# Kernel optimization log

Hardware: AMD Instinct MI355X
Metric: run time of the kernel (lower is better)

## Reference

```python
import jax, jax.numpy as jnp
import numpy as np

NUM_SPARSE = 26
VOCAB = 100000
EMB = 64
B = 2048
DENSE = 13
NUM_FEA = NUM_SPARSE + 1  # 26 embeddings + bottom-MLP output


def _xavier(key, shape):
    fan_in, fan_out = shape[0], shape[1]
    lim = jnp.sqrt(6.0 / (fan_in + fan_out))
    return jax.random.uniform(key, shape, jnp.float32, -lim, lim)


def setup_inputs() -> dict:
    key = jax.random.key(0)
    ks = jax.random.split(key, 20)
    inp = {
        "dense": jax.random.normal(ks[0], (B, DENSE), jnp.float32),
        "cat_idx": jax.random.randint(ks[1], (B, NUM_SPARSE), 0, VOCAB, jnp.int32),
        # stacked EmbeddingBag tables (all same vocab -> one [26, V, 64] tensor)
        "tables": _xavier(ks[2], (VOCAB, EMB))[None] * jnp.ones((NUM_SPARSE, 1, 1), jnp.float32) * 0
                  + jax.random.normal(ks[3], (NUM_SPARSE, VOCAB, EMB), jnp.float32) * 0.01,
        # bottom MLP: 13 -> 512 -> 256 -> 64
        "bw0": _xavier(ks[4], (DENSE, 512)), "bb0": jnp.zeros((512,), jnp.float32),
        "bw1": _xavier(ks[5], (512, 256)),   "bb1": jnp.zeros((256,), jnp.float32),
        "bw2": _xavier(ks[6], (256, EMB)),   "bb2": jnp.zeros((EMB,), jnp.float32),
        # top MLP: 415 -> 1024 -> 512 -> 256 -> 1
        "tw0": _xavier(ks[7], (EMB + NUM_FEA * (NUM_FEA - 1) // 2, 1024)), "tb0": jnp.zeros((1024,), jnp.float32),
        "tw1": _xavier(ks[8], (1024, 512)),  "tb1": jnp.zeros((512,), jnp.float32),
        "tw2": _xavier(ks[9], (512, 256)),   "tb2": jnp.zeros((256,), jnp.float32),
        "tw3": _xavier(ks[10], (256, 1)),    "tb3": jnp.zeros((1,), jnp.float32),
    }
    return inp


def reference(dense, cat_idx, tables, bw0, bb0, bw1, bb1, bw2, bb2,
              tw0, tb0, tw1, tb1, tw2, tb2, tw3, tb3):
    # bottom MLP on dense features -> [B, EMB]
    h = jax.nn.relu(dense @ bw0 + bb0)
    h = jax.nn.relu(h @ bw1 + bb1)
    bot = jax.nn.relu(h @ bw2 + bb2)

    # EmbeddingBag (single index per bag, sum mode == plain gather): [B, 26, EMB]
    feat_ids = jnp.arange(NUM_SPARSE)[None, :]  # [1, 26]
    emb = tables[feat_ids, cat_idx]             # [B, 26, EMB]

    # dot interaction: batched Gram matrix then lower-triangular gather
    T = jnp.concatenate([bot[:, None, :], emb], axis=1)  # [B, 27, EMB]
    Z = jnp.einsum("bif,bjf->bij", T, T)                  # [B, 27, 27]
    li, lj = np.tril_indices(NUM_FEA, k=-1)               # 351 pairs
    Zflat = Z[:, li, lj]                                  # [B, 351]

    R = jnp.concatenate([bot, Zflat], axis=1)             # [B, 415]

    # top MLP
    r = jax.nn.relu(R @ tw0 + tb0)
    r = jax.nn.relu(r @ tw1 + tb1)
    r = jax.nn.relu(r @ tw2 + tb2)
    out = jax.nn.sigmoid(r @ tw3 + tb3)                   # [B, 1]
    return out
```

## Files before the change

kernel.cpp:

```cpp
#include <hip/hip_runtime.h>
#include <hip/hip_bf16.h>


#define BATCH 2048
#define VOCAB 100000
#define EMB 64
#define NSPARSE 26
#define NFEA 27
#define NPAIR 351
#define RLD 448

typedef __attribute__((ext_vector_type(8))) __bf16 bf16x8;
typedef __attribute__((ext_vector_type(4))) float f32x4;
typedef __hip_bfloat16 bf16;

#define GLOAD16(g, l)                                                          \
    __builtin_amdgcn_global_load_lds(                                          \
        (const __attribute__((address_space(1))) unsigned int*)(g),            \
        (__attribute__((address_space(3))) unsigned int*)(l), 16, 0, 0)

template<int BK>
__device__ __forceinline__ int swz(int row, int s) {
    return (BK == 64) ? (s ^ (row & 7)) : (s ^ ((row >> 1) & 3));
}

template<int BK, int WR, int WC, int MREP, int NREP, bool DENSEPAD>
__global__ __launch_bounds__(256) void gemm_bf16(
    const void* __restrict__ Araw,
    const bf16* __restrict__ Wt,
    const float* __restrict__ bias,
    bf16* __restrict__ C,
    int M, int N, int K, int ldC)
{
    constexpr int BM    = WR * MREP * 16;
    constexpr int BN    = WC * NREP * 16;
    constexpr int ROWB  = BK * 2;
    constexpr int SLOTS = BK / 8;
    constexpr int KKS   = BK / 32;
    constexpr int PA    = BM * SLOTS / 256;
    constexpr int PB    = BN * SLOTS / 256;

    __shared__ __align__(16) bf16 As[BM * BK];
    __shared__ __align__(16) bf16 Bs[BN * BK];

    const int t   = threadIdx.x;
    const int nbn = N / BN;
    const int bm  = blockIdx.x / nbn;
    const int bn  = blockIdx.x % nbn;
    const int row0 = bm * BM, n0 = bn * BN;

    const int wid  = t >> 6, lane = t & 63;
    const int wr   = wid / WC, wc = wid % WC;
    const int lr   = lane & 15;
    const int q    = lane >> 4;

    const int sslot = t % SLOTS;

    const bf16* Ab[PA];
    const bf16* Bb[PB];
#pragma unroll
    for (int p = 0; p < PA; ++p) {
        const int r = (p * 256 + t) / SLOTS;
        if (!DENSEPAD)
            Ab[p] = (const bf16*)Araw + (size_t)(row0 + r) * K +
                    swz<BK>(r, sslot) * 8;
    }
#pragma unroll
    for (int p = 0; p < PB; ++p) {
        const int r = (p * 256 + t) / SLOTS;
        Bb[p] = Wt + (size_t)(n0 + r) * K + swz<BK>(r, sslot) * 8;
    }

    f32x4 acc[MREP][NREP] = {};

    for (int k0 = 0; k0 < K; k0 += BK) {
        if constexpr (DENSEPAD) {
            const float* Df = (const float*)Araw;
#pragma unroll
            for (int idx = t; idx < BM * 32; idx += 256) {
                const int r = idx >> 5, c = idx & 31;
                const float v = (c < 13) ? Df[(size_t)(row0 + r) * 13 + c] : 0.f;
                As[r * 32 + swz<BK>(r, c >> 3) * 8 + (c & 7)] =
                    __float2bfloat16(v);
            }
        } else {
#pragma unroll
            for (int p = 0; p < PA; ++p)
                GLOAD16(Ab[p] + k0, (char*)As + (p * 256 + t) * 16);
        }
#pragma unroll
        for (int p = 0; p < PB; ++p)
            GLOAD16(Bb[p] + k0, (char*)Bs + (p * 256 + t) * 16);
        __syncthreads();

        bf16x8 af[KKS][MREP], bfr[KKS][NREP];
#pragma unroll
        for (int kk = 0; kk < KKS; ++kk) {
#pragma unroll
            for (int m = 0; m < MREP; ++m) {
                const int r = wr * MREP * 16 + 16 * m + lr;
                af[kk][m] = *(const bf16x8*)((const char*)As + r * ROWB +
                                             swz<BK>(r, kk * 4 + q) * 16);
            }
#pragma unroll
            for (int n = 0; n < NREP; ++n) {
                const int r = wc * NREP * 16 + 16 * n + lr;
                bfr[kk][n] = *(const bf16x8*)((const char*)Bs + r * ROWB +
                                              swz<BK>(r, kk * 4 + q) * 16);
            }
        }
#pragma unroll
        for (int kk = 0; kk < KKS; ++kk)
#pragma unroll
            for (int m = 0; m < MREP; ++m)
#pragma unroll
                for (int n = 0; n < NREP; ++n)
                    acc[m][n] = __builtin_amdgcn_mfma_f32_16x16x32_bf16(
                        af[kk][m], bfr[kk][n], acc[m][n], 0, 0, 0);
        __syncthreads();
    }

#pragma unroll
    for (int n = 0; n < NREP; ++n) {
        const int col = n0 + wc * NREP * 16 + 16 * n + lr;
        const float bv = bias[col];
#pragma unroll
        for (int m = 0; m < MREP; ++m) {
#pragma unroll
            for (int i = 0; i < 4; ++i) {
                const int row = row0 + wr * MREP * 16 + 16 * m + q * 4 + i;
                float v = acc[m][n][i] + bv;
                v = fmaxf(v, 0.f);
                C[(size_t)row * ldC + col] = __float2bfloat16(v);
            }
        }
    }
}

struct WConvArgs {
    const float* src[6];
    bf16*        dst[6];
    int K[6], N[6], Kp[6], t0[7];
};

__global__ __launch_bounds__(256) void wconv_kernel(WConvArgs a)
{
    __shared__ float Ts[32][33];
    int w = 0;
    while (w < 5 && (int)blockIdx.x >= a.t0[w + 1]) ++w;
    const int rel = blockIdx.x - a.t0[w];
    const int K = a.K[w], N = a.N[w], Kp = a.Kp[w];
    const int nbn = N >> 5;
    const int tk = rel / nbn, tn = rel % nbn;
    const int tx = threadIdx.x & 31, ty = threadIdx.x >> 5;

    const float* src = a.src[w];
    bf16* dst = a.dst[w];

#pragma unroll
    for (int rr = 0; rr < 4; ++rr) {
        const int k = tk * 32 + ty + rr * 8;
        const int n = tn * 32 + tx;
        Ts[ty + rr * 8][tx] = (k < K) ? src[(size_t)k * N + n] : 0.f;
    }
    __syncthreads();
#pragma unroll
    for (int rr = 0; rr < 4; ++rr) {
        const int n = tn * 32 + ty + rr * 8;
        const int kp = tk * 32 + tx;
        dst[(size_t)n * Kp + kp] = __float2bfloat16(Ts[tx][ty + rr * 8]);
    }
}

__global__ __launch_bounds__(256) void interact_kernel(
    const bf16* __restrict__ h1,
    const bf16* __restrict__ bw2t,
    const float* __restrict__ bb2,
    const int* __restrict__ cat_idx,
    const float* __restrict__ tables,
    bf16* __restrict__ R)
{
    __shared__ float T[2][NFEA][EMB + 1];
    __shared__ bf16  h1s[2][256];

    const int b0 = blockIdx.x * 2;
    const int t  = threadIdx.x;

    if (t < 64) {
        const int r = t >> 5, c = (t & 31) * 8;
        *(bf16x8*)&h1s[r][c] =
            *(const bf16x8*)&h1[(size_t)(b0 + r) * 256 + c];
    }

    for (int l = t; l < 2 * NSPARSE * 16; l += 256) {
        const int r   = l / (NSPARSE * 16);
        const int rem = l % (NSPARSE * 16);
        const int j   = rem >> 4, c = (rem & 15) * 4;
        const int idx = cat_idx[(b0 + r) * NSPARSE + j];
        const float4 v =
            *(const float4*)&tables[((size_t)j * VOCAB + idx) * EMB + c];
        float* dst = &T[r][j + 1][c];
        dst[0] = v.x; dst[1] = v.y; dst[2] = v.z; dst[3] = v.w;
    }

    for (int z = t; z < 2 * (RLD - 415); z += 256) {
        const int r = z / (RLD - 415), c = z % (RLD - 415);
        R[(size_t)(b0 + r) * RLD + 415 + c] = __float2bfloat16(0.f);
    }
    __syncthreads();

    if (t < 128) {
        const int r = t >> 6, n = t & 63;
        float s = bb2[n];
        const bf16* wrow = bw2t + (size_t)n * 256;
#pragma unroll 8
        for (int k = 0; k < 256; k += 8) {
            const bf16x8 hv = *(const bf16x8*)&h1s[r][k];
            const bf16x8 wv = *(const bf16x8*)&wrow[k];
#pragma unroll
            for (int u = 0; u < 8; ++u)
                s += (float)hv[u] * (float)wv[u];
        }
        s = fmaxf(s, 0.f);
        T[r][0][n] = s;
        R[(size_t)(b0 + r) * RLD + n] = __float2bfloat16(s);
    }
    __syncthreads();

    for (int task = t; task < 2 * NPAIR; task += 256) {
        const int r = task / NPAIR, p = task % NPAIR;
        int i = (int)((1.0f + sqrtf(1.0f + 8.0f * (float)p)) * 0.5f);
        while (i * (i - 1) / 2 > p) --i;
        while ((i + 1) * i / 2 <= p) ++i;
        const int j = p - i * (i - 1) / 2;
        float s = 0.f;
#pragma unroll 16
        for (int k = 0; k < EMB; ++k) s += T[r][i][k] * T[r][j][k];
        R[(size_t)(b0 + r) * RLD + EMB + p] = __float2bfloat16(s);
    }
}

__global__ __launch_bounds__(256) void top3_kernel(
    const bf16* __restrict__ A, const float* __restrict__ w,
    const float* __restrict__ bias, float* __restrict__ out)
{
    const int gid  = blockIdx.x * 256 + threadIdx.x;
    const int row  = gid >> 6;
    const int lane = gid & 63;

    const bf16* arow = A + (size_t)row * 256;
    float s = 0.f;
#pragma unroll
    for (int k = lane; k < 256; k += 64)
        s += __bfloat162float(arow[k]) * w[k];
#pragma unroll
    for (int off = 32; off; off >>= 1) s += __shfl_down(s, off);
    if (lane == 0) out[row] = 1.f / (1.f + expf(-(s + bias[0])));
}

extern "C" void kernel_launch(void* const* d_in, const int* in_sizes, int n_in,
                              void* d_out, int out_size, void* d_ws, size_t ws_size,
                              hipStream_t stream)
{
    const float* dense   = (const float*)d_in[0];
    const int*   cat_idx = (const int*)  d_in[1];
    const float* tables  = (const float*)d_in[2];
    const float* bw0 = (const float*)d_in[3];
    const float* bb0 = (const float*)d_in[4];
    const float* bw1 = (const float*)d_in[5];
    const float* bb1 = (const float*)d_in[6];
    const float* bw2 = (const float*)d_in[7];
    const float* bb2 = (const float*)d_in[8];
    const float* tw0 = (const float*)d_in[9];
    const float* tb0 = (const float*)d_in[10];
    const float* tw1 = (const float*)d_in[11];
    const float* tb1 = (const float*)d_in[12];
    const float* tw2 = (const float*)d_in[13];
    const float* tb2 = (const float*)d_in[14];
    const float* tw3 = (const float*)d_in[15];
    const float* tb3 = (const float*)d_in[16];

    bf16* p = (bf16*)d_ws;
    bf16* h0   = p; p += (size_t)BATCH * 512;
    bf16* h1   = p; p += (size_t)BATCH * 256;
    bf16* R    = p; p += (size_t)BATCH * RLD;
    bf16* r0   = p; p += (size_t)BATCH * 1024;
    bf16* r1   = p; p += (size_t)BATCH * 512;
    bf16* r2   = p; p += (size_t)BATCH * 256;
    bf16* bw0t = p; p += 512 * 32;
    bf16* bw1t = p; p += 256 * 512;
    bf16* bw2t = p; p += 64 * 256;
    bf16* tw0t = p; p += 1024 * RLD;
    bf16* tw1t = p; p += 512 * 1024;
    bf16* tw2t = p; p += 256 * 512;
    float* out = (float*)d_out;

    WConvArgs wa;
    wa.src[0] = bw0;  wa.dst[0] = bw0t; wa.K[0] = 13;   wa.N[0] = 512;  wa.Kp[0] = 32;
    wa.src[1] = bw1;  wa.dst[1] = bw1t; wa.K[1] = 512;  wa.N[1] = 256;  wa.Kp[1] = 512;
    wa.src[2] = bw2;  wa.dst[2] = bw2t; wa.K[2] = 256;  wa.N[2] = 64;   wa.Kp[2] = 256;
    wa.src[3] = tw0;  wa.dst[3] = tw0t; wa.K[3] = 415;  wa.N[3] = 1024; wa.Kp[3] = RLD;
    wa.src[4] = tw1;  wa.dst[4] = tw1t; wa.K[4] = 1024; wa.N[4] = 512;  wa.Kp[4] = 1024;
    wa.src[5] = tw2;  wa.dst[5] = tw2t; wa.K[5] = 512;  wa.N[5] = 256;  wa.Kp[5] = 512;
    int tiles = 0;
    for (int w = 0; w < 6; ++w) {
        wa.t0[w] = tiles;
        tiles += (wa.Kp[w] >> 5) * (wa.N[w] >> 5);
    }
    wa.t0[6] = tiles;

    wconv_kernel<<<tiles, 256, 0, stream>>>(wa);

    gemm_bf16<32, 2, 2, 2, 2, true ><<<(BATCH / 64) * (512 / 64), 256, 0, stream>>>(
        dense, bw0t, bb0, h0, BATCH, 512, 32, 512);
    gemm_bf16<64, 2, 2, 2, 2, false><<<(BATCH / 64) * (256 / 64), 256, 0, stream>>>(
        h0, bw1t, bb1, h1, BATCH, 256, 512, 256);

    interact_kernel<<<BATCH / 2, 256, 0, stream>>>(
        h1, bw2t, bb2, cat_idx, tables, R);

    gemm_bf16<64, 4, 1, 2, 4, false><<<(BATCH / 128) * (1024 / 64), 256, 0, stream>>>(
        R, tw0t, tb0, r0, BATCH, 1024, RLD, 1024);
    gemm_bf16<64, 2, 2, 2, 2, false><<<(BATCH / 64) * (512 / 64), 256, 0, stream>>>(
        r0, tw1t, tb1, r1, BATCH, 512, 1024, 512);
    gemm_bf16<64, 2, 2, 2, 2, false><<<(BATCH / 64) * (256 / 64), 256, 0, stream>>>(
        r1, tw2t, tb2, r2, BATCH, 256, 512, 256);
    top3_kernel<<<BATCH / 4, 256, 0, stream>>>(r2, tw3, tb3, out);
}
```

Before: 70.29 us.

## Triple-buffer GEMM loads, move bottom layer to GEMM, split interaction per row

The bf16 GEMM now uses a three-stage LDS ring with async global-to-LDS loads and manual vmcnt waits, so loads for later k-steps overlap MFMA work. The last bottom-MLP layer moves out of the interaction kernel into a separate MFMA GEMM that writes straight into R. The interaction kernel now handles one batch row per block with coalesced per-feature gathers. The first top-layer GEMM switches to 64x64 tiles. This adds LDS use and one more launch, and the hardcoded vmcnt assumes exactly four loads per thread.

```diff
diff --git a/kernel.cpp b/kernel.cpp
--- a/kernel.cpp
+++ b/kernel.cpp
@@ -40,9 +40,6 @@
     constexpr int PA    = BM * SLOTS / 256;
     constexpr int PB    = BN * SLOTS / 256;
 
-    __shared__ __align__(16) bf16 As[BM * BK];
-    __shared__ __align__(16) bf16 Bs[BN * BK];
-
     const int t   = threadIdx.x;
     const int nbn = N / BN;
     const int bm  = blockIdx.x / nbn;
@@ -53,44 +50,27 @@
     const int wr   = wid / WC, wc = wid % WC;
     const int lr   = lane & 15;
     const int q    = lane >> 4;
-
     const int sslot = t % SLOTS;
 
-    const bf16* Ab[PA];
-    const bf16* Bb[PB];
-#pragma unroll
-    for (int p = 0; p < PA; ++p) {
-        const int r = (p * 256 + t) / SLOTS;
-        if (!DENSEPAD)
-            Ab[p] = (const bf16*)Araw + (size_t)(row0 + r) * K +
-                    swz<BK>(r, sslot) * 8;
-    }
-#pragma unroll
-    for (int p = 0; p < PB; ++p) {
-        const int r = (p * 256 + t) / SLOTS;
-        Bb[p] = Wt + (size_t)(n0 + r) * K + swz<BK>(r, sslot) * 8;
-    }
-
     f32x4 acc[MREP][NREP] = {};
 
-    for (int k0 = 0; k0 < K; k0 += BK) {
-        if constexpr (DENSEPAD) {
-            const float* Df = (const float*)Araw;
-#pragma unroll
-            for (int idx = t; idx < BM * 32; idx += 256) {
-                const int r = idx >> 5, c = idx & 31;
-                const float v = (c < 13) ? Df[(size_t)(row0 + r) * 13 + c] : 0.f;
-                As[r * 32 + swz<BK>(r, c >> 3) * 8 + (c & 7)] =
-                    __float2bfloat16(v);
-            }
-        } else {
-#pragma unroll
-            for (int p = 0; p < PA; ++p)
-                GLOAD16(Ab[p] + k0, (char*)As + (p * 256 + t) * 16);
-        }
-#pragma unroll
-        for (int p = 0; p < PB; ++p)
-            GLOAD16(Bb[p] + k0, (char*)Bs + (p * 256 + t) * 16);
+    if constexpr (DENSEPAD) {
+        __shared__ __align__(16) bf16 As[BM * BK];
+        __shared__ __align__(16) bf16 Bs[BN * BK];
+
+        const float* Df = (const float*)Araw;
+#pragma unroll
+        for (int p = 0; p < PB; ++p) {
+            const int r = (p * 256 + t) / SLOTS;
+            GLOAD16(Wt + (size_t)(n0 + r) * K + swz<BK>(r, sslot) * 8,
+                    (char*)Bs + (p * 256 + t) * 16);
+        }
+#pragma unroll
+        for (int idx = t; idx < BM * 32; idx += 256) {
+            const int r = idx >> 5, c = idx & 31;
+            const float v = (c < 13) ? Df[(size_t)(row0 + r) * 13 + c] : 0.f;
+            As[r * 32 + swz<BK>(r, c >> 3) * 8 + (c & 7)] = __float2bfloat16(v);
+        }
         __syncthreads();
 
         bf16x8 af[KKS][MREP], bfr[KKS][NREP];
@@ -117,7 +97,77 @@
                 for (int n = 0; n < NREP; ++n)
                     acc[m][n] = __builtin_amdgcn_mfma_f32_16x16x32_bf16(
                         af[kk][m], bfr[kk][n], acc[m][n], 0, 0, 0);
-        __syncthreads();
+    } else {
+        static_assert(PA + PB == 4, "vmcnt immediate assumes 4 loads/thread");
+        __shared__ __align__(16) bf16 As[3][BM * BK];
+        __shared__ __align__(16) bf16 Bs[3][BN * BK];
+
+        const bf16* Ab[PA];
+        const bf16* Bb[PB];
+#pragma unroll
+        for (int p = 0; p < PA; ++p) {
+            const int r = (p * 256 + t) / SLOTS;
+            Ab[p] = (const bf16*)Araw + (size_t)(row0 + r) * K +
+                    swz<BK>(r, sslot) * 8;
+        }
+#pragma unroll
+        for (int p = 0; p < PB; ++p) {
+            const int r = (p * 256 + t) / SLOTS;
+            Bb[p] = Wt + (size_t)(n0 + r) * K + swz<BK>(r, sslot) * 8;
+        }
+
+        const int nsteps = K / BK;
+        auto stage = [&](int s) {
+            const int buf = s % 3;
+            const int k0  = (s < nsteps ? s : nsteps - 1) * BK;
+#pragma unroll
+            for (int p = 0; p < PA; ++p)
+                GLOAD16(Ab[p] + k0, (char*)As[buf] + (p * 256 + t) * 16);
+#pragma unroll
+            for (int p = 0; p < PB; ++p)
+                GLOAD16(Bb[p] + k0, (char*)Bs[buf] + (p * 256 + t) * 16);
+        };
+
+        stage(0);
+        stage(1);
+
+        for (int ks = 0; ks < nsteps; ++ks) {
+            stage(ks + 2);
+
+            asm volatile("s_waitcnt vmcnt(8)" ::: "memory");
+            __builtin_amdgcn_s_barrier();
+            __builtin_amdgcn_sched_barrier(0);
+
+            const int buf = ks % 3;
+            bf16x8 af[KKS][MREP], bfr[KKS][NREP];
+#pragma unroll
+            for (int kk = 0; kk < KKS; ++kk) {
+#pragma unroll
+                for (int m = 0; m < MREP; ++m) {
+                    const int r = wr * MREP * 16 + 16 * m + lr;
+                    af[kk][m] = *(const bf16x8*)((const char*)As[buf] + r * ROWB +
+                                                 swz<BK>(r, kk * 4 + q) * 16);
+                }
+#pragma unroll
+                for (int n = 0; n < NREP; ++n) {
+                    const int r = wc * NREP * 16 + 16 * n + lr;
+                    bfr[kk][n] = *(const bf16x8*)((const char*)Bs[buf] + r * ROWB +
+                                                  swz<BK>(r, kk * 4 + q) * 16);
+                }
+            }
+#pragma unroll
+            for (int kk = 0; kk < KKS; ++kk)
+#pragma unroll
+                for (int m = 0; m < MREP; ++m)
+#pragma unroll
+                    for (int n = 0; n < NREP; ++n)
+                        acc[m][n] = __builtin_amdgcn_mfma_f32_16x16x32_bf16(
+                            af[kk][m], bfr[kk][n], acc[m][n], 0, 0, 0);
+
+            asm volatile("s_waitcnt lgkmcnt(0)" ::: "memory");
+            __builtin_amdgcn_s_barrier();
+            __builtin_amdgcn_sched_barrier(0);
+        }
     }
 
 #pragma unroll
@@ -173,70 +223,39 @@
 }
 
 __global__ __launch_bounds__(256) void interact_kernel(
-    const bf16* __restrict__ h1,
-    const bf16* __restrict__ bw2t,
-    const float* __restrict__ bb2,
-    const int* __restrict__ cat_idx,
-    const float* __restrict__ tables,
+    const int* __restrict__ cat_idx, const float* __restrict__ tables,
     bf16* __restrict__ R)
 {
-    __shared__ float T[2][NFEA][EMB + 1];
-    __shared__ bf16  h1s[2][256];
-
-    const int b0 = blockIdx.x * 2;
-    const int t  = threadIdx.x;
-
-    if (t < 64) {
-        const int r = t >> 5, c = (t & 31) * 8;
-        *(bf16x8*)&h1s[r][c] =
-            *(const bf16x8*)&h1[(size_t)(b0 + r) * 256 + c];
-    }
-
-    for (int l = t; l < 2 * NSPARSE * 16; l += 256) {
-        const int r   = l / (NSPARSE * 16);
-        const int rem = l % (NSPARSE * 16);
-        const int j   = rem >> 4, c = (rem & 15) * 4;
-        const int idx = cat_idx[(b0 + r) * NSPARSE + j];
-        const float4 v =
-            *(const float4*)&tables[((size_t)j * VOCAB + idx) * EMB + c];
-        float* dst = &T[r][j + 1][c];
-        dst[0] = v.x; dst[1] = v.y; dst[2] = v.z; dst[3] = v.w;
-    }
-
-    for (int z = t; z < 2 * (RLD - 415); z += 256) {
-        const int r = z / (RLD - 415), c = z % (RLD - 415);
-        R[(size_t)(b0 + r) * RLD + 415 + c] = __float2bfloat16(0.f);
+    __shared__ float T[NFEA][EMB + 1];
+
+    const int b    = blockIdx.x;
+    const int t    = threadIdx.x;
+    const int g    = t >> 6;
+    const int lane = t & 63;
+    bf16* Rrow = R + (size_t)b * RLD;
+
+    for (int f = g; f < NFEA; f += 4) {
+        if (f == 0) {
+            T[0][lane] = __bfloat162float(Rrow[lane]);
+        } else {
+            const int j   = f - 1;
+            const int idx = cat_idx[b * NSPARSE + j];
+            T[f][lane] = tables[((size_t)j * VOCAB + idx) * EMB + lane];
+        }
     }
     __syncthreads();
 
-    if (t < 128) {
-        const int r = t >> 6, n = t & 63;
-        float s = bb2[n];
-        const bf16* wrow = bw2t + (size_t)n * 256;
-#pragma unroll 8
-        for (int k = 0; k < 256; k += 8) {
-            const bf16x8 hv = *(const bf16x8*)&h1s[r][k];
-            const bf16x8 wv = *(const bf16x8*)&wrow[k];
-#pragma unroll
-            for (int u = 0; u < 8; ++u)
-                s += (float)hv[u] * (float)wv[u];
-        }
-        s = fmaxf(s, 0.f);
-        T[r][0][n] = s;
-        R[(size_t)(b0 + r) * RLD + n] = __float2bfloat16(s);
-    }
-    __syncthreads();
-
-    for (int task = t; task < 2 * NPAIR; task += 256) {
-        const int r = task / NPAIR, p = task % NPAIR;
+    if (t < RLD - 415) Rrow[415 + t] = __float2bfloat16(0.f);
+
+    for (int p = t; p < NPAIR; p += 256) {
         int i = (int)((1.0f + sqrtf(1.0f + 8.0f * (float)p)) * 0.5f);
         while (i * (i - 1) / 2 > p) --i;
         while ((i + 1) * i / 2 <= p) ++i;
         const int j = p - i * (i - 1) / 2;
         float s = 0.f;
 #pragma unroll 16
-        for (int k = 0; k < EMB; ++k) s += T[r][i][k] * T[r][j][k];
-        R[(size_t)(b0 + r) * RLD + EMB + p] = __float2bfloat16(s);
+        for (int k = 0; k < EMB; ++k) s += T[i][k] * T[j][k];
+        Rrow[EMB + p] = __float2bfloat16(s);
     }
 }
 
@@ -315,11 +334,12 @@
         dense, bw0t, bb0, h0, BATCH, 512, 32, 512);
     gemm_bf16<64, 2, 2, 2, 2, false><<<(BATCH / 64) * (256 / 64), 256, 0, stream>>>(
         h0, bw1t, bb1, h1, BATCH, 256, 512, 256);
-
-    interact_kernel<<<BATCH / 2, 256, 0, stream>>>(
-        h1, bw2t, bb2, cat_idx, tables, R);
-
-    gemm_bf16<64, 4, 1, 2, 4, false><<<(BATCH / 128) * (1024 / 64), 256, 0, stream>>>(
+    gemm_bf16<64, 2, 2, 2, 2, false><<<(BATCH / 64) * (64 / 64), 256, 0, stream>>>(
+        h1, bw2t, bb2, R, BATCH, 64, 256, RLD);
+
+    interact_kernel<<<BATCH, 256, 0, stream>>>(cat_idx, tables, R);
+
+    gemm_bf16<64, 2, 2, 2, 2, false><<<(BATCH / 64) * (1024 / 64), 256, 0, stream>>>(
         R, tw0t, tb0, r0, BATCH, 1024, RLD, 1024);
     gemm_bf16<64, 2, 2, 2, 2, false><<<(BATCH / 64) * (512 / 64), 256, 0, stream>>>(
         r0, tw1t, tb1, r1, BATCH, 512, 1024, 512);
```

Result: faster. 66.97 us (-4.7%).

## Fuse weight conversion into GEMMs, pipeline GEMM loads, fuse final layer into epilogue

Applied to the files above, without the earlier changes.

Removes the standalone weight-conversion kernel. Each weight transpose-and-convert now runs as a tail phase of the preceding kernel, and the first layer reads fp32 weights directly. Adds a triple-buffered global-to-LDS pipeline for GEMMs whose tiles fit, retiles the tw0 GEMM, and folds the final 256->1 dot product plus sigmoid into the last GEMM epilogue using LDS atomics. Together these cut launch count and expose load/compute overlap, at the cost of extra tail work in the interaction kernel and LDS atomic contention.

```diff
diff --git a/kernel.cpp b/kernel.cpp
--- a/kernel.cpp
+++ b/kernel.cpp
@@ -24,13 +24,38 @@
     return (BK == 64) ? (s ^ (row & 7)) : (s ^ ((row >> 1) & 3));
 }
 
-template<int BK, int WR, int WC, int MREP, int NREP, bool DENSEPAD>
+__device__ __forceinline__ void conv_tiles(
+    const float* __restrict__ src, bf16* __restrict__ dst,
+    int K, int N, int Kp, int tiles, int gridsz, float (*Ts)[33])
+{
+    const int tx = threadIdx.x & 31, ty = threadIdx.x >> 5;
+    for (int tile = blockIdx.x; tile < tiles; tile += gridsz) {
+        const int nbn = N >> 5;
+        const int tk = tile / nbn, tn = tile % nbn;
+        __syncthreads();
+#pragma unroll
+        for (int rr = 0; rr < 4; ++rr) {
+            const int k = tk * 32 + ty + rr * 8, n = tn * 32 + tx;
+            Ts[ty + rr * 8][tx] = (k < K) ? src[(size_t)k * N + n] : 0.f;
+        }
+        __syncthreads();
+#pragma unroll
+        for (int rr = 0; rr < 4; ++rr) {
+            const int n = tn * 32 + ty + rr * 8, kp = tk * 32 + tx;
+            dst[(size_t)n * Kp + kp] = __float2bfloat16(Ts[tx][ty + rr * 8]);
+        }
+    }
+}
+
+template<int BK, int WR, int WC, int MREP, int NREP, int MODE, bool DOCONV>
 __global__ __launch_bounds__(256) void gemm_bf16(
-    const void* __restrict__ Araw,
-    const bf16* __restrict__ Wt,
-    const float* __restrict__ bias,
-    bf16* __restrict__ C,
-    int M, int N, int K, int ldC)
+    const void* __restrict__ Araw, const void* __restrict__ Wraw,
+    const float* __restrict__ bias, bf16* __restrict__ C,
+    int M, int N, int K, int ldC,
+    const float* __restrict__ csrc, bf16* __restrict__ cdst,
+    int cK, int cN, int cKp, int cTiles,
+    const float* __restrict__ w3, const float* __restrict__ b3,
+    float* __restrict__ outv)
 {
     constexpr int BM    = WR * MREP * 16;
     constexpr int BN    = WC * NREP * 16;
@@ -39,9 +64,7 @@
     constexpr int KKS   = BK / 32;
     constexpr int PA    = BM * SLOTS / 256;
     constexpr int PB    = BN * SLOTS / 256;
-
-    __shared__ __align__(16) bf16 As[BM * BK];
-    __shared__ __align__(16) bf16 Bs[BN * BK];
+    constexpr bool PIPE = (MODE == 0) && (PA + PB == 4);
 
     const int t   = threadIdx.x;
     const int nbn = N / BN;
@@ -53,122 +76,219 @@
     const int wr   = wid / WC, wc = wid % WC;
     const int lr   = lane & 15;
     const int q    = lane >> 4;
-
     const int sslot = t % SLOTS;
 
-    const bf16* Ab[PA];
-    const bf16* Bb[PB];
-#pragma unroll
-    for (int p = 0; p < PA; ++p) {
-        const int r = (p * 256 + t) / SLOTS;
-        if (!DENSEPAD)
+    f32x4 acc[MREP][NREP] = {};
+
+    if constexpr (MODE == 1) {
+        __shared__ __align__(16) bf16 As[BM * 32];
+        __shared__ __align__(16) bf16 Bs[BN * 32];
+        const float* Df = (const float*)Araw;
+        const float* Wf = (const float*)Wraw;
+#pragma unroll
+        for (int idx = t; idx < BM * 32; idx += 256) {
+            const int r = idx >> 5, c = idx & 31;
+            const float v = (c < 13) ? Df[(size_t)(row0 + r) * 13 + c] : 0.f;
+            As[r * 32 + swz<32>(r, c >> 3) * 8 + (c & 7)] = __float2bfloat16(v);
+        }
+#pragma unroll
+        for (int idx = t; idx < BN * 32; idx += 256) {
+            const int r = idx >> 5, c = idx & 31;
+            const float v = (c < 13) ? Wf[(size_t)c * N + n0 + r] : 0.f;
+            Bs[r * 32 + swz<32>(r, c >> 3) * 8 + (c & 7)] = __float2bfloat16(v);
+        }
+        __syncthreads();
+
+        bf16x8 af[MREP], bfr[NREP];
+#pragma unroll
+        for (int m = 0; m < MREP; ++m) {
+            const int r = wr * MREP * 16 + 16 * m + lr;
+            af[m] = *(const bf16x8*)((const char*)As + r * 64 +
+                                     swz<32>(r, q) * 16);
+        }
+#pragma unroll
+        for (int n = 0; n < NREP; ++n) {
+            const int r = wc * NREP * 16 + 16 * n + lr;
+            bfr[n] = *(const bf16x8*)((const char*)Bs + r * 64 +
+                                      swz<32>(r, q) * 16);
+        }
+#pragma unroll
+        for (int m = 0; m < MREP; ++m)
+#pragma unroll
+            for (int n = 0; n < NREP; ++n)
+                acc[m][n] = __builtin_amdgcn_mfma_f32_16x16x32_bf16(
+                    af[m], bfr[n], acc[m][n], 0, 0, 0);
+        __syncthreads();
+    } else if constexpr (PIPE) {
+        __shared__ __align__(16) bf16 As[3][BM * BK];
+        __shared__ __align__(16) bf16 Bs[3][BN * BK];
+        const bf16* Wt = (const bf16*)Wraw;
+
+        const bf16* Ab[PA];
+        const bf16* Bb[PB];
+#pragma unroll
+        for (int p = 0; p < PA; ++p) {
+            const int r = (p * 256 + t) / SLOTS;
             Ab[p] = (const bf16*)Araw + (size_t)(row0 + r) * K +
                     swz<BK>(r, sslot) * 8;
-    }
-#pragma unroll
-    for (int p = 0; p < PB; ++p) {
-        const int r = (p * 256 + t) / SLOTS;
-        Bb[p] = Wt + (size_t)(n0 + r) * K + swz<BK>(r, sslot) * 8;
-    }
-
-    f32x4 acc[MREP][NREP] = {};
-
-    for (int k0 = 0; k0 < K; k0 += BK) {
-        if constexpr (DENSEPAD) {
-            const float* Df = (const float*)Araw;
-#pragma unroll
-            for (int idx = t; idx < BM * 32; idx += 256) {
-                const int r = idx >> 5, c = idx & 31;
-                const float v = (c < 13) ? Df[(size_t)(row0 + r) * 13 + c] : 0.f;
-                As[r * 32 + swz<BK>(r, c >> 3) * 8 + (c & 7)] =
-                    __float2bfloat16(v);
+        }
+#pragma unroll
+        for (int p = 0; p < PB; ++p) {
+            const int r = (p * 256 + t) / SLOTS;
+            Bb[p] = Wt + (size_t)(n0 + r) * K + swz<BK>(r, sslot) * 8;
+        }
+
+        const int nsteps = K / BK;
+        auto stage = [&](int s) {
+            const int buf = s % 3;
+            const int k0  = (s < nsteps ? s : nsteps - 1) * BK;
+#pragma unroll
+            for (int p = 0; p < PA; ++p)
+                GLOAD16(Ab[p] + k0, (char*)As[buf] + (p * 256 + t) * 16);
+#pragma unroll
+            for (int p = 0; p < PB; ++p)
+                GLOAD16(Bb[p] + k0, (char*)Bs[buf] + (p * 256 + t) * 16);
+        };
+
+        stage(0);
+        stage(1);
+
+        for (int ks = 0; ks < nsteps; ++ks) {
+            stage(ks + 2);
+
+            asm volatile("s_waitcnt vmcnt(8)" ::: "memory");
+            __builtin_amdgcn_s_barrier();
+            __builtin_amdgcn_sched_barrier(0);
+
+            const int buf = ks % 3;
+            bf16x8 af[KKS][MREP], bfr[KKS][NREP];
+#pragma unroll
+            for (int kk = 0; kk < KKS; ++kk) {
+#pragma unroll
+                for (int m = 0; m < MREP; ++m) {
+                    const int r = wr * MREP * 16 + 16 * m + lr;
+                    af[kk][m] = *(const bf16x8*)((const char*)As[buf] + r * ROWB +
+                                                 swz<BK>(r, kk * 4 + q) * 16);
+                }
+#pragma unroll
+                for (int n = 0; n < NREP; ++n) {
+                    const int r = wc * NREP * 16 + 16 * n + lr;
+                    bfr[kk][n] = *(const bf16x8*)((const char*)Bs[buf] + r * ROWB +
+                                                  swz<BK>(r, kk * 4 + q) * 16);
+                }
             }
-        } else {
+#pragma unroll
+            for (int kk = 0; kk < KKS; ++kk)
+#pragma unroll
+                for (int m = 0; m < MREP; ++m)
+#pragma unroll
+                    for (int n = 0; n < NREP; ++n)
+                        acc[m][n] = __builtin_amdgcn_mfma_f32_16x16x32_bf16(
+                            af[kk][m], bfr[kk][n], acc[m][n], 0, 0, 0);
+
+            asm volatile("s_waitcnt lgkmcnt(0)" ::: "memory");
+            __builtin_amdgcn_s_barrier();
+            __builtin_amdgcn_sched_barrier(0);
+        }
+    } else {
+        __shared__ __align__(16) bf16 As[BM * BK];
+        __shared__ __align__(16) bf16 Bs[BN * BK];
+        const bf16* Wt = (const bf16*)Wraw;
+
+        const bf16* Ab[PA];
+        const bf16* Bb[PB];
+#pragma unroll
+        for (int p = 0; p < PA; ++p) {
+            const int r = (p * 256 + t) / SLOTS;
+            Ab[p] = (const bf16*)Araw + (size_t)(row0 + r) * K +
+                    swz<BK>(r, sslot) * 8;
+        }
+#pragma unroll
+        for (int p = 0; p < PB; ++p) {
+            const int r = (p * 256 + t) / SLOTS;
+            Bb[p] = Wt + (size_t)(n0 + r) * K + swz<BK>(r, sslot) * 8;
+        }
+
+        for (int k0 = 0; k0 < K; k0 += BK) {
 #pragma unroll
             for (int p = 0; p < PA; ++p)
                 GLOAD16(Ab[p] + k0, (char*)As + (p * 256 + t) * 16);
-        }
-#pragma unroll
-        for (int p = 0; p < PB; ++p)
-            GLOAD16(Bb[p] + k0, (char*)Bs + (p * 256 + t) * 16);
-        __syncthreads();
-
-        bf16x8 af[KKS][MREP], bfr[KKS][NREP];
-#pragma unroll
-        for (int kk = 0; kk < KKS; ++kk) {
+#pragma unroll
+            for (int p = 0; p < PB; ++p)
+                GLOAD16(Bb[p] + k0, (char*)Bs + (p * 256 + t) * 16);
+            __syncthreads();
+
+            bf16x8 af[KKS][MREP], bfr[KKS][NREP];
+#pragma unroll
+            for (int kk = 0; kk < KKS; ++kk) {
+#pragma unroll
+                for (int m = 0; m < MREP; ++m) {
+                    const int r = wr * MREP * 16 + 16 * m + lr;
+                    af[kk][m] = *(const bf16x8*)((const char*)As + r * ROWB +
+                                                 swz<BK>(r, kk * 4 + q) * 16);
+                }
+#pragma unroll
+                for (int n = 0; n < NREP; ++n) {
+                    const int r = wc * NREP * 16 + 16 * n + lr;
+                    bfr[kk][n] = *(const bf16x8*)((const char*)Bs + r * ROWB +
+                                                  swz<BK>(r, kk * 4 + q) * 16);
+                }
+            }
+#pragma unroll
+            for (int kk = 0; kk < KKS; ++kk)
+#pragma unroll
+                for (int m = 0; m < MREP; ++m)
+#pragma unroll
+                    for (int n = 0; n < NREP; ++n)
+                        acc[m][n] = __builtin_amdgcn_mfma_f32_16x16x32_bf16(
+                            af[kk][m], bfr[kk][n], acc[m][n], 0, 0, 0);
+            __syncthreads();
+        }
+    }
+
+    if constexpr (MODE == 2) {
+        __shared__ float rsum[BM];
+        for (int i = t; i < BM; i += 256) rsum[i] = 0.f;
+        __syncthreads();
+#pragma unroll
+        for (int n = 0; n < NREP; ++n) {
+            const int col = n0 + wc * NREP * 16 + 16 * n + lr;
+            const float bv = bias[col];
+            const float wv = w3[col];
 #pragma unroll
             for (int m = 0; m < MREP; ++m) {
-                const int r = wr * MREP * 16 + 16 * m + lr;
-                af[kk][m] = *(const bf16x8*)((const char*)As + r * ROWB +
-                                             swz<BK>(r, kk * 4 + q) * 16);
+#pragma unroll
+                for (int i = 0; i < 4; ++i) {
+                    const int rl = wr * MREP * 16 + 16 * m + q * 4 + i;
+                    const float v = fmaxf(acc[m][n][i] + bv, 0.f);
+                    atomicAdd(&rsum[rl], v * wv);
+                }
             }
-#pragma unroll
-            for (int n = 0; n < NREP; ++n) {
-                const int r = wc * NREP * 16 + 16 * n + lr;
-                bfr[kk][n] = *(const bf16x8*)((const char*)Bs + r * ROWB +
-                                              swz<BK>(r, kk * 4 + q) * 16);
+        }
+        __syncthreads();
+        if (t < BM)
+            outv[row0 + t] = 1.f / (1.f + expf(-(rsum[t] + b3[0])));
+    } else {
+#pragma unroll
+        for (int n = 0; n < NREP; ++n) {
+            const int col = n0 + wc * NREP * 16 + 16 * n + lr;
+            const float bv = bias[col];
+#pragma unroll
+            for (int m = 0; m < MREP; ++m) {
+#pragma unroll
+                for (int i = 0; i < 4; ++i) {
+                    const int row = row0 + wr * MREP * 16 + 16 * m + q * 4 + i;
+                    float v = acc[m][n][i] + bv;
+                    v = fmaxf(v, 0.f);
+                    C[(size_t)row * ldC + col] = __float2bfloat16(v);
+                }
             }
         }
-#pragma unroll
-        for (int kk = 0; kk < KKS; ++kk)
-#pragma unroll
-            for (int m = 0; m < MREP; ++m)
-#pragma unroll
-                for (int n = 0; n < NREP; ++n)
-                    acc[m][n] = __builtin_amdgcn_mfma_f32_16x16x32_bf16(
-                        af[kk][m], bfr[kk][n], acc[m][n], 0, 0, 0);
-        __syncthreads();
-    }
-
-#pragma unroll
-    for (int n = 0; n < NREP; ++n) {
-        const int col = n0 + wc * NREP * 16 + 16 * n + lr;
-        const float bv = bias[col];
-#pragma unroll
-        for (int m = 0; m < MREP; ++m) {
-#pragma unroll
-            for (int i = 0; i < 4; ++i) {
-                const int row = row0 + wr * MREP * 16 + 16 * m + q * 4 + i;
-                float v = acc[m][n][i] + bv;
-                v = fmaxf(v, 0.f);
-                C[(size_t)row * ldC + col] = __float2bfloat16(v);
-            }
-        }
-    }
-}
-
-struct WConvArgs {
-    const float* src[6];
-    bf16*        dst[6];
-    int K[6], N[6], Kp[6], t0[7];
-};
-
-__global__ __launch_bounds__(256) void wconv_kernel(WConvArgs a)
-{
-    __shared__ float Ts[32][33];
-    int w = 0;
-    while (w < 5 && (int)blockIdx.x >= a.t0[w + 1]) ++w;
-    const int rel = blockIdx.x - a.t0[w];
-    const int K = a.K[w], N = a.N[w], Kp = a.Kp[w];
-    const int nbn = N >> 5;
-    const int tk = rel / nbn, tn = rel % nbn;
-    const int tx = threadIdx.x & 31, ty = threadIdx.x >> 5;
-
-    const float* src = a.src[w];
-    bf16* dst = a.dst[w];
-
-#pragma unroll
-    for (int rr = 0; rr < 4; ++rr) {
-        const int k = tk * 32 + ty + rr * 8;
-        const int n = tn * 32 + tx;
-        Ts[ty + rr * 8][tx] = (k < K) ? src[(size_t)k * N + n] : 0.f;
-    }
-    __syncthreads();
-#pragma unroll
-    for (int rr = 0; rr < 4; ++rr) {
-        const int n = tn * 32 + ty + rr * 8;
-        const int kp = tk * 32 + tx;
-        dst[(size_t)n * Kp + kp] = __float2bfloat16(Ts[tx][ty + rr * 8]);
+    }
+
+    if constexpr (DOCONV) {
+        __shared__ float Ts[32][33];
+        conv_tiles(csrc, cdst, cK, cN, cKp, cTiles, gridDim.x, Ts);
     }
 }
 
@@ -178,10 +298,14 @@
     const float* __restrict__ bb2,
     const int* __restrict__ cat_idx,
     const float* __restrict__ tables,
-    bf16* __restrict__ R)
+    bf16* __restrict__ R,
+    const float* __restrict__ tw0, bf16* __restrict__ tw0t,
+    const float* __restrict__ tw1, bf16* __restrict__ tw1t,
+    const float* __restrict__ tw2, bf16* __restrict__ tw2t)
 {
     __shared__ float T[2][NFEA][EMB + 1];
     __shared__ bf16  h1s[2][256];
+    __shared__ float Ts[32][33];
 
     const int b0 = blockIdx.x * 2;
     const int t  = threadIdx.x;
@@ -238,24 +362,10 @@
         for (int k = 0; k < EMB; ++k) s += T[r][i][k] * T[r][j][k];
         R[(size_t)(b0 + r) * RLD + EMB + p] = __float2bfloat16(s);
     }
-}
-
-__global__ __launch_bounds__(256) void top3_kernel(
-    const bf16* __restrict__ A, const float* __restrict__ w,
-    const float* __restrict__ bias, float* __restrict__ out)
-{
-    const int gid  = blockIdx.x * 256 + threadIdx.x;
-    const int row  = gid >> 6;
-    const int lane = gid & 63;
-
-    const bf16* arow = A + (size_t)row * 256;
-    float s = 0.f;
-#pragma unroll
-    for (int k = lane; k < 256; k += 64)
-        s += __bfloat162float(arow[k]) * w[k];
-#pragma unroll
-    for (int off = 32; off; off >>= 1) s += __shfl_down(s, off);
-    if (lane == 0) out[row] = 1.f / (1.f + expf(-(s + bias[0])));
+
+    conv_tiles(tw0, tw0t, 415,  1024, RLD,  (RLD >> 5) * (1024 >> 5), gridDim.x, Ts);
+    conv_tiles(tw1, tw1t, 1024, 512,  1024, (1024 >> 5) * (512 >> 5), gridDim.x, Ts);
+    conv_tiles(tw2, tw2t, 512,  256,  512,  (512 >> 5) * (256 >> 5),  gridDim.x, Ts);
 }
 
 extern "C" void kernel_launch(void* const* d_in, const int* in_sizes, int n_in,
@@ -286,8 +396,6 @@
     bf16* R    = p; p += (size_t)BATCH * RLD;
     bf16* r0   = p; p += (size_t)BATCH * 1024;
     bf16* r1   = p; p += (size_t)BATCH * 512;
-    bf16* r2   = p; p += (size_t)BATCH * 256;
-    bf16* bw0t = p; p += 512 * 32;
     bf16* bw1t = p; p += 256 * 512;
     bf16* bw2t = p; p += 64 * 256;
     bf16* tw0t = p; p += 1024 * RLD;
@@ -295,35 +403,34 @@
     bf16* tw2t = p; p += 256 * 512;
     float* out = (float*)d_out;
 
-    WConvArgs wa;
-    wa.src[0] = bw0;  wa.dst[0] = bw0t; wa.K[0] = 13;   wa.N[0] = 512;  wa.Kp[0] = 32;
-    wa.src[1] = bw1;  wa.dst[1] = bw1t; wa.K[1] = 512;  wa.N[1] = 256;  wa.Kp[1] = 512;
-    wa.src[2] = bw2;  wa.dst[2] = bw2t; wa.K[2] = 256;  wa.N[2] = 64;   wa.Kp[2] = 256;
-    wa.src[3] = tw0;  wa.dst[3] = tw0t; wa.K[3] = 415;  wa.N[3] = 1024; wa.Kp[3] = RLD;
-    wa.src[4] = tw1;  wa.dst[4] = tw1t; wa.K[4] = 1024; wa.N[4] = 512;  wa.Kp[4] = 1024;
-    wa.src[5] = tw2;  wa.dst[5] = tw2t; wa.K[5] = 512;  wa.N[5] = 256;  wa.Kp[5] = 512;
-    int tiles = 0;
-    for (int w = 0; w < 6; ++w) {
-        wa.t0[w] = tiles;
-        tiles += (wa.Kp[w] >> 5) * (wa.N[w] >> 5);
-    }
-    wa.t0[6] = tiles;
-
-    wconv_kernel<<<tiles, 256, 0, stream>>>(wa);
-
-    gemm_bf16<32, 2, 2, 2, 2, true ><<<(BATCH / 64) * (512 / 64), 256, 0, stream>>>(
-        dense, bw0t, bb0, h0, BATCH, 512, 32, 512);
-    gemm_bf16<64, 2, 2, 2, 2, false><<<(BATCH / 64) * (256 / 64), 256, 0, stream>>>(
-        h0, bw1t, bb1, h1, BATCH, 256, 512, 256);
+    gemm_bf16<32, 2, 2, 2, 2, 1, true>
+        <<<(BATCH / 64) * (512 / 64), 256, 0, stream>>>(
+        dense, bw0, bb0, h0, BATCH, 512, 32, 512,
+        bw1, bw1t, 512, 256, 512, (512 >> 5) * (256 >> 5),
+        nullptr, nullptr, nullptr);
+
+    gemm_bf16<64, 2, 2, 2, 2, 0, true>
+        <<<(BATCH / 64) * (256 / 64), 256, 0, stream>>>(
+        h0, bw1t, bb1, h1, BATCH, 256, 512, 256,
+        bw2, bw2t, 256, 64, 256, (256 >> 5) * (64 >> 5),
+        nullptr, nullptr, nullptr);
 
     interact_kernel<<<BATCH / 2, 256, 0, stream>>>(
-        h1, bw2t, bb2, cat_idx, tables, R);
-
-    gemm_bf16<64, 4, 1, 2, 4, false><<<(BATCH / 128) * (1024 / 64), 256, 0, stream>>>(
-        R, tw0t, tb0, r0, BATCH, 1024, RLD, 1024);
-    gemm_bf16<64, 2, 2, 2, 2, false><<<(BATCH / 64) * (512 / 64), 256, 0, stream>>>(
-        r0, tw1t, tb1, r1, BATCH, 512, 1024, 512);
-    gemm_bf16<64, 2, 2, 2, 2, false><<<(BATCH / 64) * (256 / 64), 256, 0, stream>>>(
-        r1, tw2t, tb2, r2, BATCH, 256, 512, 256);
-    top3_kernel<<<BATCH / 4, 256, 0, stream>>>(r2, tw3, tb3, out);
+        h1, bw2t, bb2, cat_idx, tables, R,
+        tw0, tw0t, tw1, tw1t, tw2, tw2t);
+
+    gemm_bf16<64, 2, 2, 2, 2, 0, false>
+        <<<(BATCH / 64) * (1024 / 64), 256, 0, stream>>>(
+        R, tw0t, tb0, r0, BATCH, 1024, RLD, 1024,
+        nullptr, nullptr, 0, 0, 0, 0, nullptr, nullptr, nullptr);
+
+    gemm_bf16<64, 2, 2, 2, 2, 0, false>
+        <<<(BATCH / 64) * (512 / 64), 256, 0, stream>>>(
+        r0, tw1t, tb1, r1, BATCH, 512, 1024, 512,
+        nullptr, nullptr, 0, 0, 0, 0, nullptr, nullptr, nullptr);
+
+    gemm_bf16<64, 1, 4, 2, 4, 2, false>
+        <<<(BATCH / 32) * (256 / 256), 256, 0, stream>>>(
+        r1, tw2t, tb2, nullptr, BATCH, 256, 512, 256,
+        nullptr, nullptr, 0, 0, 0, 0, tw3, tb3, out);
 }
```

New measurement: 82.36 us. 1.17x slower.
